# Performance work log

Hardware: AMD Instinct MI355X
Metric: run time of the kernel (lower is better)

## Reference

```python
import jax, jax.numpy as jnp
import numpy as np

P_DROP = 0.6  # dropout prob from the source module
N_NODES = 50000
N_EDGES = 800000


def _cheb_edge_weights(edge_index, num_nodes):
    # ChebConv with sym normalization and default lambda_max=2.0:
    # scaled Laplacian hat(L) = 2L/lambda_max - I = -D^{-1/2} A D^{-1/2}
    # (diagonal becomes 0), so edge weight = -1/sqrt(deg[row]*deg[col]).
    row, col = edge_index[0], edge_index[1]
    deg = jnp.zeros((num_nodes,), jnp.float32).at[row].add(1.0)
    dis = jnp.where(deg > 0, jax.lax.rsqrt(jnp.maximum(deg, 1.0)), 0.0)
    return -dis[row] * dis[col]


def _prop(x, row, col, w, n):
    # hat(L) @ x via gather-scale-scatter over the edge list
    return jnp.zeros((n, x.shape[1]), x.dtype).at[row].add(w[:, None] * x[col])


def _cheb_conv(x, row, col, w, W, b, n):
    # Chebyshev recursion: Tx0 = x, Tx1 = hat(L) x, Tx_k = 2 hat(L) Tx_{k-1} - Tx_{k-2}
    Tx0 = x
    out = Tx0 @ W[0]
    Tx1 = _prop(Tx0, row, col, w, n)
    out = out + Tx1 @ W[1]
    for k in range(2, W.shape[0]):
        Tx2 = 2.0 * _prop(Tx1, row, col, w, n) - Tx0
        out = out + Tx2 @ W[k]
        Tx0, Tx1 = Tx1, Tx2
    return out + b


def _dropout(x, key, p):
    keep = jax.random.bernoulli(key, 1.0 - p, x.shape)
    return jnp.where(keep, x * (1.0 / (1.0 - p)), 0.0)


def setup_inputs() -> dict:
    key = jax.random.key(0)
    ks = jax.random.split(key, 8)
    x = jax.random.normal(ks[0], (N_NODES, 64), jnp.float32)
    edge_index = jax.random.randint(ks[1], (2, N_EDGES), 0, N_NODES, jnp.int64)
    W0 = jax.random.normal(ks[2], (2, 64, 64), jnp.float32) * 0.1
    b0 = jnp.zeros((64,), jnp.float32)
    W1 = jax.random.normal(ks[3], (2, 64, 64), jnp.float32) * 0.1
    b1 = jnp.zeros((64,), jnp.float32)
    W2 = jax.random.normal(ks[4], (2, 64, 32), jnp.float32) * 0.1
    b2 = jnp.zeros((32,), jnp.float32)
    return {"x": x, "edge_index": edge_index, "W0": W0, "b0": b0,
            "W1": W1, "b1": b1, "W2": W2, "b2": b2}


def reference(x, edge_index, W0, b0, W1, b1, W2, b2):
    row, col = edge_index[0], edge_index[1]
    n = x.shape[0]
    w = _cheb_edge_weights(edge_index, n)
    dkey = jax.random.key(1)
    params = [(W0, b0), (W1, b1), (W2, b2)]
    for i, (W, b) in enumerate(params):
        x = _dropout(x, jax.random.fold_in(dkey, i), P_DROP)
        x = _cheb_conv(x, row, col, w, W, b, n)
        if i < len(params) - 1:
            x = jax.nn.relu(x)
    return x
```

## Files before the change

kernel.cpp:

```cpp
#include <hip/hip_runtime.h>
#include <stdint.h>

typedef _Float16 half8 __attribute__((ext_vector_type(8)));
typedef float float4v __attribute__((ext_vector_type(4)));

__host__ __device__ inline void tf2x32(uint32_t k0, uint32_t k1,
                                       uint32_t x0, uint32_t x1,
                                       uint32_t* o0, uint32_t* o1) {
  const uint32_t ks2 = k0 ^ k1 ^ 0x1BD11BDAu;
#define ROTL(v, s) (((v) << (s)) | ((v) >> (32 - (s))))
#define RND(r) do { x0 += x1; x1 = ROTL(x1, r); x1 ^= x0; } while (0)
  x0 += k0; x1 += k1;
  RND(13); RND(15); RND(26); RND(6);
  x0 += k1; x1 += ks2 + 1u;
  RND(17); RND(29); RND(16); RND(24);
  x0 += ks2; x1 += k0 + 2u;
  RND(13); RND(15); RND(26); RND(6);
  x0 += k0; x1 += k1 + 3u;
  RND(17); RND(29); RND(16); RND(24);
  x0 += k1; x1 += ks2 + 4u;
  RND(13); RND(15); RND(26); RND(6);
  x0 += ks2; x1 += k0 + 5u;
  *o0 = x0; *o1 = x1;
#undef RND
#undef ROTL
}

__device__ inline bool drop_keep(uint32_t k0, uint32_t k1, uint32_t idx) {
  uint32_t o0, o1;
  tf2x32(k0, k1, 0u, idx, &o0, &o1);
  uint32_t bits = o0 ^ o1;
  float u = __uint_as_float((bits >> 9) | 0x3f800000u) - 1.0f;
  return u < 0.4f;
}

__global__ void k_fill2(const int* __restrict__ row, const int* __restrict__ col,
                        int* __restrict__ cnt, uint16_t* __restrict__ cs,
                        int e, int rows_per_xcd) {
  const int owner = blockIdx.x & 7;
  const int i = (blockIdx.x >> 3) * 256 + threadIdx.x;
  if (i < e) {
    int r = row[i];
    if (r / rows_per_xcd == owner) {
      int pos = atomicAdd(&cnt[r], 1);
      if (pos < 64) cs[(r << 6) + pos] = (uint16_t)col[i];
    }
  }
}

__global__ void k_drop(const float* __restrict__ x, const int* __restrict__ cnt,
                       uint16_t* __restrict__ cs, float* __restrict__ dis,
                       _Float16* __restrict__ y, _Float16* __restrict__ ys,
                       _Float16* __restrict__ ysb, uint32_t k0, uint32_t k1,
                       int n, int nd,
                       const float* __restrict__ W0, const float* __restrict__ W1,
                       const float* __restrict__ W2, _Float16* __restrict__ wh) {
  int i = blockIdx.x * 256 + threadIdx.x;
  if (i < 20480) {
    int d = i;
    if (d < 8192) {
      int o = d >> 7, k = d & 127;
      wh[d] = (_Float16)W0[k * 64 + o];
    } else if (d < 16384) {
      int d1 = d - 8192, o = d1 >> 7, k = d1 & 127;
      wh[d] = (_Float16)W1[k * 64 + o];
    } else {
      int d2 = d - 16384, o = d2 >> 7, k = d2 & 127;
      wh[d] = (_Float16)W2[k * 32 + o];
    }
  }
  if (i < 64) {
    ys[((size_t)n << 6) + i]  = (_Float16)0.f;
    ysb[((size_t)n << 6) + i] = (_Float16)0.f;
  }
  if (i < nd) {
    const int r = i >> 6;
    const int t = i & 63;
    const int d = cnt[r];
    const float dis_r = (d > 0) ? rsqrtf((float)d) : 0.0f;
    float v = drop_keep(k0, k1, (uint32_t)i) ? x[i] * 2.5f : 0.0f;
    y[i]  = (_Float16)v;
    ys[i] = (_Float16)(dis_r * v);
    if (t == 0) dis[r] = dis_r;
    const int cn = d < 64 ? d : 64;
    const int rnd = (cn + 7) & ~7;
    if (t >= cn && t < rnd) cs[(r << 6) + t] = (uint16_t)n;
  }
}

template<int COUT, bool RELU, bool DROPN, bool WBF>
__global__ __launch_bounds__(256, 8) void k_conv(
    const _Float16* __restrict__ yg, const _Float16* __restrict__ ysg,
    const int* __restrict__ cnt, const uint16_t* __restrict__ cs,
    const float* __restrict__ dis, const _Float16* __restrict__ wt,
    const float* __restrict__ b, float* __restrict__ outf,
    _Float16* __restrict__ outb, _Float16* __restrict__ outs,
    uint32_t nk0, uint32_t nk1, int n) {
  constexpr int R  = 16;
  constexpr int TS = 136;
  __shared__ __align__(16) _Float16 xp[R][TS];

  const int wave = threadIdx.x >> 6;
  const int t    = threadIdx.x & 63;
  const int row0 = blockIdx.x * R;

  for (int i = 0; i < 4; ++i) {
    const int rl = wave * 4 + i;
    const int r  = row0 + rl;
    if (r < n) {
      float acc = 0.0f;
      const int d   = cnt[r];
      const int cn  = d < 64 ? d : 64;
      const int rnd = (cn + 7) & ~7;
      const int base = r << 6;
      for (int j = 0; j < rnd; j += 8) {
        const uint4 cc = *(const uint4*)&cs[base + j];
        uint32_t c[8];
        c[0] = cc.x & 0xffffu; c[1] = cc.x >> 16;
        c[2] = cc.y & 0xffffu; c[3] = cc.y >> 16;
        c[4] = cc.z & 0xffffu; c[5] = cc.z >> 16;
        c[6] = cc.w & 0xffffu; c[7] = cc.w >> 16;
        _Float16 xv[8];
        #pragma unroll
        for (int k = 0; k < 8; ++k) xv[k] = ysg[(c[k] << 6) + t];
        #pragma unroll
        for (int k = 0; k < 8; ++k) acc += (float)xv[k];
      }
      xp[rl][t]      = yg[(uint32_t)(r << 6) + t];
      xp[rl][64 + t] = (_Float16)(-dis[r] * acc);
    }
  }
  __syncthreads();

  constexpr int NW = COUT / 16;
  const int nn   = t & 15;
  const int quad = t >> 4;
  if (wave < NW) {
    const int colg = wave * 16 + nn;
    float4v acc = {0.f, 0.f, 0.f, 0.f};
    #pragma unroll
    for (int ks = 0; ks < 4; ++ks) {
      half8 a  = *(const half8*)&xp[nn][quad * 8 + 32 * ks];
      half8 bb = *(const half8*)&wt[(size_t)colg * 128 + quad * 8 + 32 * ks];
      acc = __builtin_amdgcn_mfma_f32_16x16x32_f16(a, bb, acc, 0, 0, 0);
    }
    const float bias = b[colg];
    #pragma unroll
    for (int rg = 0; rg < 4; ++rg) {
      const int rl = quad * 4 + rg;
      const int rr = row0 + rl;
      if (rr < n) {
        float v = acc[rg] + bias;
        if (RELU) v = fmaxf(v, 0.0f);
        if (DROPN) {
          if (drop_keep(nk0, nk1, (uint32_t)(rr * 64 + colg))) v *= 2.5f;
          else v = 0.0f;
        }
        if (WBF) {
          outb[(size_t)rr * COUT + colg] = (_Float16)v;
          outs[(size_t)rr * COUT + colg] = (_Float16)(dis[rr] * v);
        } else {
          outf[(size_t)rr * COUT + colg] = v;
        }
      }
    }
  }
}

extern "C" void kernel_launch(void* const* d_in, const int* in_sizes, int n_in,
                              void* d_out, int out_size, void* d_ws, size_t ws_size,
                              hipStream_t stream) {
  const float* x   = (const float*)d_in[0];
  const int*   ei  = (const int*)d_in[1];
  const float* W0  = (const float*)d_in[2];
  const float* b0  = (const float*)d_in[3];
  const float* W1f = (const float*)d_in[4];
  const float* b1  = (const float*)d_in[5];
  const float* W2  = (const float*)d_in[6];
  const float* b2  = (const float*)d_in[7];
  float* out = (float*)d_out;

  const int n = in_sizes[0] / 64;
  const int e = in_sizes[1] / 2;
  const int* row = ei;
  const int* col = ei + e;

  size_t off = 0;
  auto carve = [&](size_t elems) {
    size_t o = off;
    off += (elems + 255) & ~(size_t)255;
    return o;
  };
  int* base = (int*)d_ws;
  int*      cnt = base + carve(n);
  float*    dis = (float*)(base + carve(n));
  uint16_t* cs  = (uint16_t*)(base + carve((size_t)n * 32));
  _Float16* ya  = (_Float16*)(base + carve((size_t)n * 32));
  _Float16* ysa = (_Float16*)(base + carve((size_t)(n + 1) * 32));
  _Float16* yb  = (_Float16*)(base + carve((size_t)n * 32));
  _Float16* ysb = (_Float16*)(base + carve((size_t)(n + 1) * 32));
  _Float16* wh  = (_Float16*)(base + carve(10240));
  (void)ws_size;
  _Float16* wh0 = wh;
  _Float16* wh1 = wh + 8192;
  _Float16* wh2 = wh + 16384;

  uint32_t dk[3][2];
  for (uint32_t i = 0; i < 3; ++i) tf2x32(0u, 1u, 0u, i, &dk[i][0], &dk[i][1]);

  hipMemsetAsync(cnt, 0, (size_t)n * 4, stream);

  const int nchunk = (e + 255) / 256;
  const int bd = ((n * 64) + 255) / 256;
  const int bc = (n + 15) / 16;
  const int rpx = (n + 7) / 8;

  k_fill2<<<nchunk * 8, 256, 0, stream>>>(row, col, cnt, cs, e, rpx);
  k_drop<<<bd, 256, 0, stream>>>(x, cnt, cs, dis, ya, ysa, ysb,
                                 dk[0][0], dk[0][1], n, n * 64,
                                 W0, W1f, W2, wh);

  k_conv<64, true,  true,  true ><<<bc, 256, 0, stream>>>(
      ya, ysa, cnt, cs, dis, wh0, b0, nullptr, yb, ysb, dk[1][0], dk[1][1], n);
  k_conv<64, true,  true,  true ><<<bc, 256, 0, stream>>>(
      yb, ysb, cnt, cs, dis, wh1, b1, nullptr, ya, ysa, dk[2][0], dk[2][1], n);
  k_conv<32, false, false, false><<<bc, 256, 0, stream>>>(
      ya, ysa, cnt, cs, dis, wh2, b2, out, nullptr, nullptr, 0u, 0u, n);
}
```

Baseline: 222.8 us.

## Vectorize neighbor gather with 16-byte loads and in-wave LDS reduction

The neighbor gather changes shape. Before, each lane loaded one fp16 feature per neighbor. Now each group of 8 lanes takes one neighbor and each lane loads 8 features as a 16-byte vector. Neighbor indices are loaded once per row and broadcast with shuffles. The gather is specialized by degree bucket (16/32/64), and partial sums are reduced across neighbor groups through a per-wave LDS buffer. The aim is fewer, wider memory instructions and more loads in flight per row. The cost is extra LDS use and shuffle work, and the launch-bounds occupancy hint drops from 8 to 6.

```diff
diff --git a/kernel.cpp b/kernel.cpp
--- a/kernel.cpp
+++ b/kernel.cpp
@@ -88,8 +88,25 @@
   }
 }
 
+template<int T>
+__device__ __forceinline__ void gatherT(int idx_all, int rnd, int g, int sub,
+                                        const _Float16* __restrict__ ysg,
+                                        uint32_t dummy, float acc[8]) {
+  half8 hv[T];
+  #pragma unroll
+  for (int j = 0; j < T; ++j) {
+    int sh = __shfl(idx_all, j * 8 + g, 64);
+    uint32_t c = (j * 8 < rnd) ? (uint32_t)(sh & 0xffff) : dummy;
+    hv[j] = *(const half8*)((const char*)ysg + (c << 7) + (sub << 4));
+  }
+  #pragma unroll
+  for (int j = 0; j < T; ++j)
+    #pragma unroll
+    for (int k = 0; k < 8; ++k) acc[k] += (float)hv[j][k];
+}
+
 template<int COUT, bool RELU, bool DROPN, bool WBF>
-__global__ __launch_bounds__(256, 8) void k_conv(
+__global__ __launch_bounds__(256, 6) void k_conv(
     const _Float16* __restrict__ yg, const _Float16* __restrict__ ysg,
     const int* __restrict__ cnt, const uint16_t* __restrict__ cs,
     const float* __restrict__ dis, const _Float16* __restrict__ wt,
@@ -99,35 +116,37 @@
   constexpr int R  = 16;
   constexpr int TS = 136;
   __shared__ __align__(16) _Float16 xp[R][TS];
+  __shared__ float red[4][8][72];
 
   const int wave = threadIdx.x >> 6;
   const int t    = threadIdx.x & 63;
   const int row0 = blockIdx.x * R;
+  const int g    = t >> 3;
+  const int sub  = t & 7;
+  const uint32_t dummy = (uint32_t)n;
 
   for (int i = 0; i < 4; ++i) {
     const int rl = wave * 4 + i;
     const int r  = row0 + rl;
     if (r < n) {
-      float acc = 0.0f;
-      const int d   = cnt[r];
-      const int cn  = d < 64 ? d : 64;
-      const int rnd = (cn + 7) & ~7;
+      const int d    = cnt[r];
+      const int cn   = d < 64 ? d : 64;
+      const int rnd  = (cn + 7) & ~7;
       const int base = r << 6;
-      for (int j = 0; j < rnd; j += 8) {
-        const uint4 cc = *(const uint4*)&cs[base + j];
-        uint32_t c[8];
-        c[0] = cc.x & 0xffffu; c[1] = cc.x >> 16;
-        c[2] = cc.y & 0xffffu; c[3] = cc.y >> 16;
-        c[4] = cc.z & 0xffffu; c[5] = cc.z >> 16;
-        c[6] = cc.w & 0xffffu; c[7] = cc.w >> 16;
-        _Float16 xv[8];
-        #pragma unroll
-        for (int k = 0; k < 8; ++k) xv[k] = ysg[(c[k] << 6) + t];
-        #pragma unroll
-        for (int k = 0; k < 8; ++k) acc += (float)xv[k];
-      }
+      const int idx_all = cs[base + t];
+      float acc[8] = {0.f, 0.f, 0.f, 0.f, 0.f, 0.f, 0.f, 0.f};
+      if (rnd <= 16)      gatherT<2>(idx_all, rnd, g, sub, ysg, dummy, acc);
+      else if (rnd <= 32) gatherT<4>(idx_all, rnd, g, sub, ysg, dummy, acc);
+      else                gatherT<8>(idx_all, rnd, g, sub, ysg, dummy, acc);
+      #pragma unroll
+      for (int k = 0; k < 8; ++k) red[wave][k][t] = acc[k];
+      __builtin_amdgcn_wave_barrier();
+      float s = 0.f;
+      #pragma unroll
+      for (int g2 = 0; g2 < 8; ++g2) s += red[wave][sub][8 * g2 + g];
+      __builtin_amdgcn_wave_barrier();
       xp[rl][t]      = yg[(uint32_t)(r << 6) + t];
-      xp[rl][64 + t] = (_Float16)(-dis[r] * acc);
+      xp[rl][64 + t] = (_Float16)(-dis[r] * s);
     }
   }
   __syncthreads();
```

New measurement: 193.5 us. 13.1% less time.
